# Performance work log

Measured on AMD Instinct MI355X. Metric: run time of the kernel, lower is better.

## Reference

```python
import jax, jax.numpy as jnp
import numpy as np

B, L, H, R, T = 2, 128, 768, 4, 3


def setup_inputs() -> dict:
    key = jax.random.key(0)
    ks = jax.random.split(key, 10)
    s = lambda k, shape: jax.random.normal(k, shape, dtype=jnp.float32) * 0.02
    return {
        "hidden_state": jax.random.normal(ks[0], (B, L, H), dtype=jnp.float32),
        "W_src": s(ks[1], (R * H, H)),
        "b_src": s(ks[2], (R * H,)),
        "W_tgt": s(ks[3], (R * H, H)),
        "b_tgt": s(ks[4], (R * H,)),
        "w_out": s(ks[5], (H,)),
        "dense_W": s(ks[6], (T * H, H)),
        "dense_b": s(ks[7], (T * H,)),
        "clf_W": s(ks[8], (1, H)),
        "clf_b": s(ks[9], (1,)),
    }


def reference(hidden_state, W_src, b_src, W_tgt, b_tgt, w_out,
              dense_W, dense_b, clf_W, clf_b):
    b, l, h = hidden_state.shape
    # Biaffine pairwise relation scoring (dropout = identity at eval).
    h_src = (hidden_state @ W_src.T + b_src).reshape(b, l, R, h)  # [B,L,R,H]
    h_tgt = (hidden_state @ W_tgt.T + b_tgt).reshape(b, l, R, h)  # [B,L,R,H]
    # Pairwise broadcast-add -> tanh -> reduce with w_out. [B,L,L,R,H] intermediate.
    pair = jnp.tanh(h_src[:, :, None, :, :] + h_tgt[:, None, :, :, :])
    relation_logits = jnp.einsum('bstrh,h->bstr', pair, w_out)
    relation_logits = jnp.transpose(relation_logits, (0, 3, 1, 2))  # [B,R,L,L]
    # Token binary classification head.
    z = (hidden_state @ dense_W.T + dense_b).reshape(b, l, T, h)   # [B,L,T,H]
    source_mask_logits = jnp.tanh(z) @ clf_W[0] + clf_b[0]          # [B,L,T]
    source_mask_logits = jnp.transpose(source_mask_logits, (0, 2, 1))  # [B,T,L]
    return relation_logits, source_mask_logits, h_src, h_tgt
```

## Files before the change

### kernel.cpp

```cpp
#include <hip/hip_runtime.h>
#include <hip/hip_bf16.h>

#define LL 128
#define HH 768
#define OFF_REL  0
#define OFF_MASK 131072
#define OFF_HSRC 131840
#define OFF_HTGT 918272
#define SCALEC 2.8853900817779268f

typedef __attribute__((ext_vector_type(8))) short short8;
typedef __attribute__((ext_vector_type(4))) float floatx4;

__device__ inline unsigned short f2bf(float f) {
  unsigned u = __float_as_uint(f);
  u += 0x7FFFu + ((u >> 16) & 1u);
  return (unsigned short)(u >> 16);
}
struct us4 { unsigned short x, y, z, w; };

__global__ __launch_bounds__(256) void cvt_kernel(
    const float4* __restrict__ hs, const float4* __restrict__ wsrc,
    const float4* __restrict__ wtgt, const float4* __restrict__ wd,
    us4* __restrict__ ab, us4* __restrict__ wb)
{
  const int n0 = 49152;
  const int n1 = n0 + 589824;
  const int n2 = n1 + 589824;
  const int n3 = n2 + 442368;
  int stride = gridDim.x * blockDim.x;
  for (int i = blockIdx.x * blockDim.x + threadIdx.x; i < n3; i += stride) {
    const float4* src; us4* dst;
    if (i < n0)      { src = hs   + i;        dst = ab + i; }
    else if (i < n1) { src = wsrc + (i - n0); dst = wb + (i - n0); }
    else if (i < n2) { src = wtgt + (i - n1); dst = wb + 589824 + (i - n1); }
    else             { src = wd   + (i - n2); dst = wb + 1179648 + (i - n2); }
    float4 v = *src;
    us4 o; o.x = f2bf(v.x); o.y = f2bf(v.y); o.z = f2bf(v.z); o.w = f2bf(v.w);
    *dst = o;
  }
}

__global__ __launch_bounds__(256, 4) void gemm_kernel(
    const unsigned short* __restrict__ Ab, const unsigned short* __restrict__ Wb,
    const float* __restrict__ b_src, const float* __restrict__ b_tgt,
    const float* __restrict__ dense_b,
    float* __restrict__ out, float* __restrict__ z,
    float* __restrict__ Es, float* __restrict__ Et)
{
  __shared__ unsigned short sA[2][64][72];
  __shared__ unsigned short sB[2][64][72];
  int tid = threadIdx.x;
  int wave = tid >> 6, lane = tid & 63;
  int nb = blockIdx.x, rb = blockIdx.y;
  int gcol0 = nb * 64;
  int grow0 = rb * 64;

  int s_row = tid >> 3, s_slot = (tid & 7) * 8;
  const unsigned short* gA0 = Ab + (long)(grow0 + s_row) * HH + s_slot;
  const unsigned short* gA1 = gA0 + 32 * HH;
  const unsigned short* gB0 = Wb + (long)(gcol0 + s_row) * HH + s_slot;
  const unsigned short* gB1 = gB0 + 32 * HH;

  int lr = lane & 15, lk8 = (lane >> 4) * 8;
  int wm = (wave >> 1) * 32, wn = (wave & 1) * 32;

  floatx4 acc[2][2];
  #pragma unroll
  for (int mi = 0; mi < 2; ++mi)
    #pragma unroll
    for (int ni = 0; ni < 2; ++ni)
      acc[mi][ni] = (floatx4){0.f, 0.f, 0.f, 0.f};

  {
    uint4 a0 = *(const uint4*)(gA0);
    uint4 a1 = *(const uint4*)(gA1);
    uint4 b0 = *(const uint4*)(gB0);
    uint4 b1 = *(const uint4*)(gB1);
    *(uint4*)&sA[0][s_row][s_slot]      = a0;
    *(uint4*)&sA[0][s_row + 32][s_slot] = a1;
    *(uint4*)&sB[0][s_row][s_slot]      = b0;
    *(uint4*)&sB[0][s_row + 32][s_slot] = b1;
  }
  __syncthreads();

  #pragma unroll 2
  for (int kt = 0; kt < 12; ++kt) {
    int c = kt & 1;
    uint4 na0, na1, nb0, nb1;
    if (kt < 11) {
      int off = (kt + 1) * 64;
      na0 = *(const uint4*)(gA0 + off);
      na1 = *(const uint4*)(gA1 + off);
      nb0 = *(const uint4*)(gB0 + off);
      nb1 = *(const uint4*)(gB1 + off);
    }
    #pragma unroll
    for (int ks = 0; ks < 2; ++ks) {
      short8 fa0 = *(const short8*)&sA[c][wm + lr][ks * 32 + lk8];
      short8 fa1 = *(const short8*)&sA[c][wm + 16 + lr][ks * 32 + lk8];
      short8 fb0 = *(const short8*)&sB[c][wn + lr][ks * 32 + lk8];
      short8 fb1 = *(const short8*)&sB[c][wn + 16 + lr][ks * 32 + lk8];
      acc[0][0] = __builtin_amdgcn_mfma_f32_16x16x32_bf16(fa0, fb0, acc[0][0], 0, 0, 0);
      acc[0][1] = __builtin_amdgcn_mfma_f32_16x16x32_bf16(fa0, fb1, acc[0][1], 0, 0, 0);
      acc[1][0] = __builtin_amdgcn_mfma_f32_16x16x32_bf16(fa1, fb0, acc[1][0], 0, 0, 0);
      acc[1][1] = __builtin_amdgcn_mfma_f32_16x16x32_bf16(fa1, fb1, acc[1][1], 0, 0, 0);
    }
    if (kt < 11) {
      *(uint4*)&sA[c ^ 1][s_row][s_slot]      = na0;
      *(uint4*)&sA[c ^ 1][s_row + 32][s_slot] = na1;
      *(uint4*)&sB[c ^ 1][s_row][s_slot]      = nb0;
      *(uint4*)&sB[c ^ 1][s_row + 32][s_slot] = nb1;
    }
    __syncthreads();
  }

  int lrow = (lane >> 4) * 4;
  #pragma unroll
  for (int mi = 0; mi < 2; ++mi)
  #pragma unroll
  for (int ni = 0; ni < 2; ++ni) {
    int colg = gcol0 + wn + ni * 16 + lr;
    int row0 = grow0 + wm + mi * 16 + lrow;
    if (nb < 48) {
      float bv = b_src[colg];
      #pragma unroll
      for (int r2 = 0; r2 < 4; ++r2) {
        int row = row0 + r2;
        float v = acc[mi][ni][r2] + bv;
        out[OFF_HSRC + row * 3072 + colg] = v;
        Es[row * 3072 + colg] = __builtin_amdgcn_exp2f(SCALEC * v);
      }
    } else if (nb < 96) {
      int cc = colg - 3072;
      float bv = b_tgt[cc];
      #pragma unroll
      for (int r2 = 0; r2 < 4; ++r2) {
        int row = row0 + r2;
        float v = acc[mi][ni][r2] + bv;
        out[OFF_HTGT + row * 3072 + cc] = v;
        Et[row * 3072 + cc] = __builtin_amdgcn_exp2f(SCALEC * v);
      }
    } else {
      int cc = colg - 6144;
      float bv = dense_b[cc];
      #pragma unroll
      for (int r2 = 0; r2 < 4; ++r2)
        z[(row0 + r2) * 2304 + cc] = acc[mi][ni][r2] + bv;
    }
  }
}

#define PHC 256
__global__ __launch_bounds__(512) void pair_kernel(
    const float* __restrict__ Es, const float* __restrict__ Et,
    const float* __restrict__ w_out,
    const float* __restrict__ z, const float* __restrict__ clf_W,
    const float* __restrict__ clf_b, float* __restrict__ out)
{
  int tid = threadIdx.x;

  if (blockIdx.z == 8) {
    int blk = blockIdx.y * 8 + blockIdx.x;
    int wave = tid >> 6, lane = tid & 63;
    int slot = blk * 8 + wave;
    for (int o = slot; o < 768; o += 512) {
      int b = o / 384, rem = o - b * 384;
      int t = rem >> 7, lt = rem & 127;
      const float* zr = z + (long)(b * LL + lt) * 2304 + t * HH;
      float acc = 0.f;
      for (int h = lane; h < HH; h += 64) {
        float x = zr[h];
        float th = 1.f - 2.f * __builtin_amdgcn_rcpf(1.f + __builtin_amdgcn_exp2f(SCALEC * x));
        acc = fmaf(clf_W[h], th, acc);
      }
      #pragma unroll
      for (int d = 32; d; d >>= 1) acc += __shfl_down(acc, d);
      if (lane == 0) out[OFF_MASK + o] = acc + clf_b[0];
    }
    return;
  }

  __shared__ float sA[16][PHC + 4];
  __shared__ float sB[16][PHC + 4];
  __shared__ float sRed[2048];
  __shared__ float sWsum;

  int g = tid >> 6, lane = tid & 63;
  int sq = lane >> 3, tq = lane & 7;
  int t0 = blockIdx.x * 16, s0 = blockIdx.y * 16;
  int br = blockIdx.z, bb = br >> 2, r = br & 3;

  if (tid < 64) {
    float wsm = 0.f;
    for (int h = tid; h < HH; h += 64) wsm += w_out[h];
    #pragma unroll
    for (int d = 32; d; d >>= 1) wsm += __shfl_down(wsm, d);
    if (tid == 0) sWsum = wsm;
  }

  float a00 = 0.f, a01 = 0.f, a10 = 0.f, a11 = 0.f;

  for (int c = 0; c < HH; c += PHC) {
    int offu = __builtin_amdgcn_readfirstlane(c + g * 32);
    float4 wv[8];
    #pragma unroll
    for (int q = 0; q < 8; ++q) wv[q] = *(const float4*)(w_out + offu + q * 4);

    __syncthreads();
    #pragma unroll
    for (int j = 0; j < 2; ++j) {
      int idx = tid * 2 + j;
      int row = idx >> 6, col4 = (idx & 63) * 4;
      *(float4*)&sA[row][col4] =
          *(const float4*)(Es + (long)(bb * LL + s0 + row) * 3072 + r * HH + c + col4);
      *(float4*)&sB[row][col4] =
          *(const float4*)(Et + (long)(bb * LL + t0 + row) * 3072 + r * HH + c + col4);
    }
    __syncthreads();

    const float* pA0 = &sA[2 * sq][g * 32];
    const float* pA1 = &sA[2 * sq + 1][g * 32];
    const float* pB0 = &sB[2 * tq][g * 32];
    const float* pB1 = &sB[2 * tq + 1][g * 32];
    #pragma unroll
    for (int hh = 0; hh < 32; hh += 4) {
      float4 e0 = *(const float4*)(pA0 + hh);
      float4 e1 = *(const float4*)(pA1 + hh);
      float4 f0 = *(const float4*)(pB0 + hh);
      float4 f1 = *(const float4*)(pB1 + hh);
      float4 vw = wv[hh >> 2];
      a00 = fmaf(vw.x, __builtin_amdgcn_rcpf(fmaf(e0.x, f0.x, 1.f)), a00);
      a01 = fmaf(vw.x, __builtin_amdgcn_rcpf(fmaf(e0.x, f1.x, 1.f)), a01);
      a10 = fmaf(vw.x, __builtin_amdgcn_rcpf(fmaf(e1.x, f0.x, 1.f)), a10);
      a11 = fmaf(vw.x, __builtin_amdgcn_rcpf(fmaf(e1.x, f1.x, 1.f)), a11);
      a00 = fmaf(vw.y, __builtin_amdgcn_rcpf(fmaf(e0.y, f0.y, 1.f)), a00);
      a01 = fmaf(vw.y, __builtin_amdgcn_rcpf(fmaf(e0.y, f1.y, 1.f)), a01);
      a10 = fmaf(vw.y, __builtin_amdgcn_rcpf(fmaf(e1.y, f0.y, 1.f)), a10);
      a11 = fmaf(vw.y, __builtin_amdgcn_rcpf(fmaf(e1.y, f1.y, 1.f)), a11);
      a00 = fmaf(vw.z, __builtin_amdgcn_rcpf(fmaf(e0.z, f0.z, 1.f)), a00);
      a01 = fmaf(vw.z, __builtin_amdgcn_rcpf(fmaf(e0.z, f1.z, 1.f)), a01);
      a10 = fmaf(vw.z, __builtin_amdgcn_rcpf(fmaf(e1.z, f0.z, 1.f)), a10);
      a11 = fmaf(vw.z, __builtin_amdgcn_rcpf(fmaf(e1.z, f1.z, 1.f)), a11);
      a00 = fmaf(vw.w, __builtin_amdgcn_rcpf(fmaf(e0.w, f0.w, 1.f)), a00);
      a01 = fmaf(vw.w, __builtin_amdgcn_rcpf(fmaf(e0.w, f1.w, 1.f)), a01);
      a10 = fmaf(vw.w, __builtin_amdgcn_rcpf(fmaf(e1.w, f0.w, 1.f)), a10);
      a11 = fmaf(vw.w, __builtin_amdgcn_rcpf(fmaf(e1.w, f1.w, 1.f)), a11);
    }
  }

  sRed[0 * 512 + g * 64 + lane] = a00;
  sRed[1 * 512 + g * 64 + lane] = a01;
  sRed[2 * 512 + g * 64 + lane] = a10;
  sRed[3 * 512 + g * 64 + lane] = a11;
  __syncthreads();
  if (tid < 256) {
    int s = tid >> 4, t = tid & 15;
    int pp = (s >> 1) * 8 + (t >> 1);
    int sl = (s & 1) * 2 + (t & 1);
    float sum = 0.f;
    #pragma unroll
    for (int gg = 0; gg < 8; ++gg) sum += sRed[sl * 512 + gg * 64 + pp];
    out[((long)br * LL + (s0 + s)) * LL + (t0 + t)] = sWsum - 2.f * sum;
  }
}

extern "C" void kernel_launch(void* const* d_in, const int* in_sizes, int n_in,
                              void* d_out, int out_size, void* d_ws, size_t ws_size,
                              hipStream_t stream)
{
  const float* hidden  = (const float*)d_in[0];
  const float* W_src   = (const float*)d_in[1];
  const float* b_src   = (const float*)d_in[2];
  const float* W_tgt   = (const float*)d_in[3];
  const float* b_tgt   = (const float*)d_in[4];
  const float* w_out   = (const float*)d_in[5];
  const float* dense_W = (const float*)d_in[6];
  const float* dense_b = (const float*)d_in[7];
  const float* clf_W   = (const float*)d_in[8];
  const float* clf_b   = (const float*)d_in[9];
  float* out = (float*)d_out;
  char* ws = (char*)d_ws;

  unsigned short* Ab = (unsigned short*)ws;
  unsigned short* Wb = (unsigned short*)(ws + 393216);
  float* z  = (float*)(ws + 13369344);
  float* Es = (float*)(ws + 15728640);
  float* Et = (float*)(ws + 18874368);

  hipLaunchKernelGGL(cvt_kernel, dim3(2048), dim3(256), 0, stream,
      (const float4*)hidden, (const float4*)W_src, (const float4*)W_tgt,
      (const float4*)dense_W, (us4*)Ab, (us4*)Wb);
  hipLaunchKernelGGL(gemm_kernel, dim3(132, 4), dim3(256), 0, stream,
      Ab, Wb, b_src, b_tgt, dense_b, out, z, Es, Et);
  hipLaunchKernelGGL(pair_kernel, dim3(8, 8, 9), dim3(512), 0, stream,
      Es, Et, w_out, z, clf_W, clf_b, out + OFF_REL);
}
```

Measured before the change: 44.63 us.

## Fuse fp32-to-bf16 conversion into GEMM tile loads, drop the separate convert kernel

Removes the standalone conversion kernel that wrote bf16 copies of the hidden state and all three weight matrices. The GEMM now reads fp32 directly from global memory and converts to bf16 while staging tiles into shared memory. This saves a launch and a full extra write and read of about 13 MB of weights. In exchange each GEMM tile load moves twice as many bytes and holds more registers for the prefetched fp32 values, which may affect occupancy. The hidden-state rows are also reconverted by every column block.

```diff
diff --git a/kernel.cpp b/kernel.cpp
--- a/kernel.cpp
+++ b/kernel.cpp
@@ -12,37 +12,19 @@
 typedef __attribute__((ext_vector_type(8))) short short8;
 typedef __attribute__((ext_vector_type(4))) float floatx4;
 
-__device__ inline unsigned short f2bf(float f) {
-  unsigned u = __float_as_uint(f);
-  u += 0x7FFFu + ((u >> 16) & 1u);
-  return (unsigned short)(u >> 16);
-}
-struct us4 { unsigned short x, y, z, w; };
-
-__global__ __launch_bounds__(256) void cvt_kernel(
-    const float4* __restrict__ hs, const float4* __restrict__ wsrc,
-    const float4* __restrict__ wtgt, const float4* __restrict__ wd,
-    us4* __restrict__ ab, us4* __restrict__ wb)
-{
-  const int n0 = 49152;
-  const int n1 = n0 + 589824;
-  const int n2 = n1 + 589824;
-  const int n3 = n2 + 442368;
-  int stride = gridDim.x * blockDim.x;
-  for (int i = blockIdx.x * blockDim.x + threadIdx.x; i < n3; i += stride) {
-    const float4* src; us4* dst;
-    if (i < n0)      { src = hs   + i;        dst = ab + i; }
-    else if (i < n1) { src = wsrc + (i - n0); dst = wb + (i - n0); }
-    else if (i < n2) { src = wtgt + (i - n1); dst = wb + 589824 + (i - n1); }
-    else             { src = wd   + (i - n2); dst = wb + 1179648 + (i - n2); }
-    float4 v = *src;
-    us4 o; o.x = f2bf(v.x); o.y = f2bf(v.y); o.z = f2bf(v.z); o.w = f2bf(v.w);
-    *dst = o;
-  }
+__device__ __forceinline__ uint4 cvt8(float4 lo, float4 hi) {
+  union { __hip_bfloat162 h2[4]; uint4 u4; } u;
+  u.h2[0] = __float22bfloat162_rn(float2{lo.x, lo.y});
+  u.h2[1] = __float22bfloat162_rn(float2{lo.z, lo.w});
+  u.h2[2] = __float22bfloat162_rn(float2{hi.x, hi.y});
+  u.h2[3] = __float22bfloat162_rn(float2{hi.z, hi.w});
+  return u.u4;
 }
 
 __global__ __launch_bounds__(256, 4) void gemm_kernel(
-    const unsigned short* __restrict__ Ab, const unsigned short* __restrict__ Wb,
+    const float* __restrict__ hidden,
+    const float* __restrict__ Wsrc, const float* __restrict__ Wtgt,
+    const float* __restrict__ Wd,
     const float* __restrict__ b_src, const float* __restrict__ b_tgt,
     const float* __restrict__ dense_b,
     float* __restrict__ out, float* __restrict__ z,
@@ -56,11 +38,16 @@
   int gcol0 = nb * 64;
   int grow0 = rb * 64;
 
+  const float* W; int wrow0; int which;
+  if (nb < 48)      { W = Wsrc; wrow0 = gcol0;        which = 0; }
+  else if (nb < 96) { W = Wtgt; wrow0 = gcol0 - 3072; which = 1; }
+  else              { W = Wd;   wrow0 = gcol0 - 6144; which = 2; }
+
   int s_row = tid >> 3, s_slot = (tid & 7) * 8;
-  const unsigned short* gA0 = Ab + (long)(grow0 + s_row) * HH + s_slot;
-  const unsigned short* gA1 = gA0 + 32 * HH;
-  const unsigned short* gB0 = Wb + (long)(gcol0 + s_row) * HH + s_slot;
-  const unsigned short* gB1 = gB0 + 32 * HH;
+  const float* gA0 = hidden + (long)(grow0 + s_row) * HH + s_slot;
+  const float* gA1 = gA0 + 32 * HH;
+  const float* gB0 = W + (long)(wrow0 + s_row) * HH + s_slot;
+  const float* gB1 = gB0 + 32 * HH;
 
   int lr = lane & 15, lk8 = (lane >> 4) * 8;
   int wm = (wave >> 1) * 32, wn = (wave & 1) * 32;
@@ -73,27 +60,27 @@
       acc[mi][ni] = (floatx4){0.f, 0.f, 0.f, 0.f};
 
   {
-    uint4 a0 = *(const uint4*)(gA0);
-    uint4 a1 = *(const uint4*)(gA1);
-    uint4 b0 = *(const uint4*)(gB0);
-    uint4 b1 = *(const uint4*)(gB1);
-    *(uint4*)&sA[0][s_row][s_slot]      = a0;
-    *(uint4*)&sA[0][s_row + 32][s_slot] = a1;
-    *(uint4*)&sB[0][s_row][s_slot]      = b0;
-    *(uint4*)&sB[0][s_row + 32][s_slot] = b1;
+    float4 a0l = *(const float4*)(gA0),     a0h = *(const float4*)(gA0 + 4);
+    float4 a1l = *(const float4*)(gA1),     a1h = *(const float4*)(gA1 + 4);
+    float4 b0l = *(const float4*)(gB0),     b0h = *(const float4*)(gB0 + 4);
+    float4 b1l = *(const float4*)(gB1),     b1h = *(const float4*)(gB1 + 4);
+    *(uint4*)&sA[0][s_row][s_slot]      = cvt8(a0l, a0h);
+    *(uint4*)&sA[0][s_row + 32][s_slot] = cvt8(a1l, a1h);
+    *(uint4*)&sB[0][s_row][s_slot]      = cvt8(b0l, b0h);
+    *(uint4*)&sB[0][s_row + 32][s_slot] = cvt8(b1l, b1h);
   }
   __syncthreads();
 
   #pragma unroll 2
   for (int kt = 0; kt < 12; ++kt) {
     int c = kt & 1;
-    uint4 na0, na1, nb0, nb1;
+    float4 na0l, na0h, na1l, na1h, nb0l, nb0h, nb1l, nb1h;
     if (kt < 11) {
       int off = (kt + 1) * 64;
-      na0 = *(const uint4*)(gA0 + off);
-      na1 = *(const uint4*)(gA1 + off);
-      nb0 = *(const uint4*)(gB0 + off);
-      nb1 = *(const uint4*)(gB1 + off);
+      na0l = *(const float4*)(gA0 + off); na0h = *(const float4*)(gA0 + off + 4);
+      na1l = *(const float4*)(gA1 + off); na1h = *(const float4*)(gA1 + off + 4);
+      nb0l = *(const float4*)(gB0 + off); nb0h = *(const float4*)(gB0 + off + 4);
+      nb1l = *(const float4*)(gB1 + off); nb1h = *(const float4*)(gB1 + off + 4);
     }
     #pragma unroll
     for (int ks = 0; ks < 2; ++ks) {
@@ -107,10 +94,10 @@
       acc[1][1] = __builtin_amdgcn_mfma_f32_16x16x32_bf16(fa1, fb1, acc[1][1], 0, 0, 0);
     }
     if (kt < 11) {
-      *(uint4*)&sA[c ^ 1][s_row][s_slot]      = na0;
-      *(uint4*)&sA[c ^ 1][s_row + 32][s_slot] = na1;
-      *(uint4*)&sB[c ^ 1][s_row][s_slot]      = nb0;
-      *(uint4*)&sB[c ^ 1][s_row + 32][s_slot] = nb1;
+      *(uint4*)&sA[c ^ 1][s_row][s_slot]      = cvt8(na0l, na0h);
+      *(uint4*)&sA[c ^ 1][s_row + 32][s_slot] = cvt8(na1l, na1h);
+      *(uint4*)&sB[c ^ 1][s_row][s_slot]      = cvt8(nb0l, nb0h);
+      *(uint4*)&sB[c ^ 1][s_row + 32][s_slot] = cvt8(nb1l, nb1h);
     }
     __syncthreads();
   }
@@ -122,7 +109,7 @@
   for (int ni = 0; ni < 2; ++ni) {
     int colg = gcol0 + wn + ni * 16 + lr;
     int row0 = grow0 + wm + mi * 16 + lrow;
-    if (nb < 48) {
+    if (which == 0) {
       float bv = b_src[colg];
       #pragma unroll
       for (int r2 = 0; r2 < 4; ++r2) {
@@ -131,7 +118,7 @@
         out[OFF_HSRC + row * 3072 + colg] = v;
         Es[row * 3072 + colg] = __builtin_amdgcn_exp2f(SCALEC * v);
       }
-    } else if (nb < 96) {
+    } else if (which == 1) {
       int cc = colg - 3072;
       float bv = b_tgt[cc];
       #pragma unroll
@@ -282,17 +269,12 @@
   float* out = (float*)d_out;
   char* ws = (char*)d_ws;
 
-  unsigned short* Ab = (unsigned short*)ws;
-  unsigned short* Wb = (unsigned short*)(ws + 393216);
-  float* z  = (float*)(ws + 13369344);
-  float* Es = (float*)(ws + 15728640);
-  float* Et = (float*)(ws + 18874368);
-
-  hipLaunchKernelGGL(cvt_kernel, dim3(2048), dim3(256), 0, stream,
-      (const float4*)hidden, (const float4*)W_src, (const float4*)W_tgt,
-      (const float4*)dense_W, (us4*)Ab, (us4*)Wb);
+  float* z  = (float*)(ws);
+  float* Es = (float*)(ws + 2359296);
+  float* Et = (float*)(ws + 5505024);
+
   hipLaunchKernelGGL(gemm_kernel, dim3(132, 4), dim3(256), 0, stream,
-      Ab, Wb, b_src, b_tgt, dense_b, out, z, Es, Et);
+      hidden, W_src, W_tgt, dense_W, b_src, b_tgt, dense_b, out, z, Es, Et);
   hipLaunchKernelGGL(pair_kernel, dim3(8, 8, 9), dim3(512), 0, stream,
       Es, Et, w_out, z, clf_W, clf_b, out + OFF_REL);
 }
```

Measured after the change: 44.39 us. No clear change (-0.5%).

## Use direct global-to-LDS loads and 128-row tiles in projection GEMM

Applied to the files above, without the earlier changes.

Rewrites the projection GEMM to stage A and B tiles with global_load_lds, which writes global memory straight into shared memory without passing through registers. The M tile grows from 64 to 128 rows and the K step shrinks to 32, so each wave computes a 64x32 output with eight MFMAs per step and the grid halves to 132x2 blocks. The goal is to cut register traffic and redundant weight loads. In exchange the LDS layout is unpadded (64-byte rows), which may cause bank conflicts, the loop needs twice as many barriers, and fewer blocks may leave CUs idle.

```diff
diff --git a/kernel.cpp b/kernel.cpp
--- a/kernel.cpp
+++ b/kernel.cpp
@@ -18,6 +18,13 @@
   return (unsigned short)(u >> 16);
 }
 struct us4 { unsigned short x, y, z, w; };
+
+__device__ __forceinline__ void gload16(const void* g, void* l) {
+  __builtin_amdgcn_global_load_lds(
+      (const __attribute__((address_space(1))) unsigned int*)g,
+      (__attribute__((address_space(3))) unsigned int*)l,
+      16, 0, 0);
+}
 
 __global__ __launch_bounds__(256) void cvt_kernel(
     const float4* __restrict__ hs, const float4* __restrict__ wsrc,
@@ -48,96 +55,87 @@
     float* __restrict__ out, float* __restrict__ z,
     float* __restrict__ Es, float* __restrict__ Et)
 {
-  __shared__ unsigned short sA[2][64][72];
-  __shared__ unsigned short sB[2][64][72];
+  __shared__ __align__(1024) unsigned short sAB[2][6144];
   int tid = threadIdx.x;
   int wave = tid >> 6, lane = tid & 63;
-  int nb = blockIdx.x, rb = blockIdx.y;
+  int nb = blockIdx.x;
+  int mb = blockIdx.y * 128;
+
+  int which = (nb < 48) ? 0 : (nb < 96) ? 1 : 2;
   int gcol0 = nb * 64;
-  int grow0 = rb * 64;
-
-  int s_row = tid >> 3, s_slot = (tid & 7) * 8;
-  const unsigned short* gA0 = Ab + (long)(grow0 + s_row) * HH + s_slot;
-  const unsigned short* gA1 = gA0 + 32 * HH;
-  const unsigned short* gB0 = Wb + (long)(gcol0 + s_row) * HH + s_slot;
-  const unsigned short* gB1 = gB0 + 32 * HH;
-
-  int lr = lane & 15, lk8 = (lane >> 4) * 8;
-  int wm = (wave >> 1) * 32, wn = (wave & 1) * 32;
-
-  floatx4 acc[2][2];
+
+  int srowA = wave * 16 + (lane >> 2);
+  int sslot = (lane & 3) * 8;
+  const unsigned short* gA = Ab + (long)(mb + srowA) * HH + sslot;
+  const unsigned short* gB = Wb + (long)(gcol0 + srowA) * HH + sslot;
+
+  int lr = lane & 15;
+  int lk16 = (lane >> 4) * 16;
+  int wm = (wave >> 1) * 64, wn = (wave & 1) * 32;
+
+  floatx4 acc[4][2];
   #pragma unroll
-  for (int mi = 0; mi < 2; ++mi)
-    #pragma unroll
-    for (int ni = 0; ni < 2; ++ni)
-      acc[mi][ni] = (floatx4){0.f, 0.f, 0.f, 0.f};
-
-  {
-    uint4 a0 = *(const uint4*)(gA0);
-    uint4 a1 = *(const uint4*)(gA1);
-    uint4 b0 = *(const uint4*)(gB0);
-    uint4 b1 = *(const uint4*)(gB1);
-    *(uint4*)&sA[0][s_row][s_slot]      = a0;
-    *(uint4*)&sA[0][s_row + 32][s_slot] = a1;
-    *(uint4*)&sB[0][s_row][s_slot]      = b0;
-    *(uint4*)&sB[0][s_row + 32][s_slot] = b1;
-  }
+  for (int fi = 0; fi < 4; ++fi)
+    #pragma unroll
+    for (int fj = 0; fj < 2; ++fj)
+      acc[fi][fj] = (floatx4){0.f, 0.f, 0.f, 0.f};
+
+#define STAGE(BUF, KT) do {                                              \
+    char* base = (char*)&sAB[BUF][0];                                    \
+    gload16(gA + (KT) * 32,            base + wave * 1024);              \
+    gload16(gA + 64 * HH + (KT) * 32,  base + 4096 + wave * 1024);       \
+    gload16(gB + (KT) * 32,            base + 8192 + wave * 1024);       \
+  } while (0)
+
+  STAGE(0, 0);
   __syncthreads();
 
   #pragma unroll 2
-  for (int kt = 0; kt < 12; ++kt) {
-    int c = kt & 1;
-    uint4 na0, na1, nb0, nb1;
-    if (kt < 11) {
-      int off = (kt + 1) * 64;
-      na0 = *(const uint4*)(gA0 + off);
-      na1 = *(const uint4*)(gA1 + off);
-      nb0 = *(const uint4*)(gB0 + off);
-      nb1 = *(const uint4*)(gB1 + off);
-    }
-    #pragma unroll
-    for (int ks = 0; ks < 2; ++ks) {
-      short8 fa0 = *(const short8*)&sA[c][wm + lr][ks * 32 + lk8];
-      short8 fa1 = *(const short8*)&sA[c][wm + 16 + lr][ks * 32 + lk8];
-      short8 fb0 = *(const short8*)&sB[c][wn + lr][ks * 32 + lk8];
-      short8 fb1 = *(const short8*)&sB[c][wn + 16 + lr][ks * 32 + lk8];
-      acc[0][0] = __builtin_amdgcn_mfma_f32_16x16x32_bf16(fa0, fb0, acc[0][0], 0, 0, 0);
-      acc[0][1] = __builtin_amdgcn_mfma_f32_16x16x32_bf16(fa0, fb1, acc[0][1], 0, 0, 0);
-      acc[1][0] = __builtin_amdgcn_mfma_f32_16x16x32_bf16(fa1, fb0, acc[1][0], 0, 0, 0);
-      acc[1][1] = __builtin_amdgcn_mfma_f32_16x16x32_bf16(fa1, fb1, acc[1][1], 0, 0, 0);
-    }
-    if (kt < 11) {
-      *(uint4*)&sA[c ^ 1][s_row][s_slot]      = na0;
-      *(uint4*)&sA[c ^ 1][s_row + 32][s_slot] = na1;
-      *(uint4*)&sB[c ^ 1][s_row][s_slot]      = nb0;
-      *(uint4*)&sB[c ^ 1][s_row + 32][s_slot] = nb1;
-    }
+  for (int kt = 0; kt < 24; ++kt) {
+    int cur = kt & 1;
+    if (kt < 23) STAGE(cur ^ 1, kt + 1);
+    const char* base = (const char*)&sAB[cur][0];
+    short8 af0 = *(const short8*)(base + (wm + lr) * 64 + lk16);
+    short8 af1 = *(const short8*)(base + (wm + 16 + lr) * 64 + lk16);
+    short8 af2 = *(const short8*)(base + (wm + 32 + lr) * 64 + lk16);
+    short8 af3 = *(const short8*)(base + (wm + 48 + lr) * 64 + lk16);
+    short8 bf0 = *(const short8*)(base + 8192 + (wn + lr) * 64 + lk16);
+    short8 bf1 = *(const short8*)(base + 8192 + (wn + 16 + lr) * 64 + lk16);
+    acc[0][0] = __builtin_amdgcn_mfma_f32_16x16x32_bf16(af0, bf0, acc[0][0], 0, 0, 0);
+    acc[0][1] = __builtin_amdgcn_mfma_f32_16x16x32_bf16(af0, bf1, acc[0][1], 0, 0, 0);
+    acc[1][0] = __builtin_amdgcn_mfma_f32_16x16x32_bf16(af1, bf0, acc[1][0], 0, 0, 0);
+    acc[1][1] = __builtin_amdgcn_mfma_f32_16x16x32_bf16(af1, bf1, acc[1][1], 0, 0, 0);
+    acc[2][0] = __builtin_amdgcn_mfma_f32_16x16x32_bf16(af2, bf0, acc[2][0], 0, 0, 0);
+    acc[2][1] = __builtin_amdgcn_mfma_f32_16x16x32_bf16(af2, bf1, acc[2][1], 0, 0, 0);
+    acc[3][0] = __builtin_amdgcn_mfma_f32_16x16x32_bf16(af3, bf0, acc[3][0], 0, 0, 0);
+    acc[3][1] = __builtin_amdgcn_mfma_f32_16x16x32_bf16(af3, bf1, acc[3][1], 0, 0, 0);
     __syncthreads();
   }
+#undef STAGE
 
   int lrow = (lane >> 4) * 4;
   #pragma unroll
-  for (int mi = 0; mi < 2; ++mi)
+  for (int fi = 0; fi < 4; ++fi)
   #pragma unroll
-  for (int ni = 0; ni < 2; ++ni) {
-    int colg = gcol0 + wn + ni * 16 + lr;
-    int row0 = grow0 + wm + mi * 16 + lrow;
-    if (nb < 48) {
+  for (int fj = 0; fj < 2; ++fj) {
+    int colg = gcol0 + wn + fj * 16 + lr;
+    int row0 = mb + wm + fi * 16 + lrow;
+    if (which == 0) {
       float bv = b_src[colg];
       #pragma unroll
       for (int r2 = 0; r2 < 4; ++r2) {
         int row = row0 + r2;
-        float v = acc[mi][ni][r2] + bv;
+        float v = acc[fi][fj][r2] + bv;
         out[OFF_HSRC + row * 3072 + colg] = v;
         Es[row * 3072 + colg] = __builtin_amdgcn_exp2f(SCALEC * v);
       }
-    } else if (nb < 96) {
+    } else if (which == 1) {
       int cc = colg - 3072;
       float bv = b_tgt[cc];
       #pragma unroll
       for (int r2 = 0; r2 < 4; ++r2) {
         int row = row0 + r2;
-        float v = acc[mi][ni][r2] + bv;
+        float v = acc[fi][fj][r2] + bv;
         out[OFF_HTGT + row * 3072 + cc] = v;
         Et[row * 3072 + cc] = __builtin_amdgcn_exp2f(SCALEC * v);
       }
@@ -146,7 +144,7 @@
       float bv = dense_b[cc];
       #pragma unroll
       for (int r2 = 0; r2 < 4; ++r2)
-        z[(row0 + r2) * 2304 + cc] = acc[mi][ni][r2] + bv;
+        z[(row0 + r2) * 2304 + cc] = acc[fi][fj][r2] + bv;
     }
   }
 }
@@ -291,7 +289,7 @@
   hipLaunchKernelGGL(cvt_kernel, dim3(2048), dim3(256), 0, stream,
       (const float4*)hidden, (const float4*)W_src, (const float4*)W_tgt,
       (const float4*)dense_W, (us4*)Ab, (us4*)Wb);
-  hipLaunchKernelGGL(gemm_kernel, dim3(132, 4), dim3(256), 0, stream,
+  hipLaunchKernelGGL(gemm_kernel, dim3(132, 2), dim3(256), 0, stream,
       Ab, Wb, b_src, b_tgt, dense_b, out, z, Es, Et);
   hipLaunchKernelGGL(pair_kernel, dim3(8, 8, 9), dim3(512), 0, stream,
       Es, Et, w_out, z, clf_W, clf_b, out + OFF_REL);
```

Result: slower. 46.36 us (+3.9%).

## Load MFMA fragments directly from global memory, dropping LDS staging in GEMM

Applied to the files above, without the earlier changes.

Drops the shared-memory double-buffered tiles from the projection GEMM. Each wave now loads its bf16 A/B fragments straight from global memory into registers with a one-step register prefetch. This removes LDS writes and reads plus block barriers. In exchange, data shared between waves is no longer reused through LDS, so global/L2 traffic rises (each fragment row is fetched by two waves) and the 16-byte per-lane row-strided loads are less coalesced.

```diff
diff --git a/kernel.cpp b/kernel.cpp
--- a/kernel.cpp
+++ b/kernel.cpp
@@ -48,23 +48,21 @@
     float* __restrict__ out, float* __restrict__ z,
     float* __restrict__ Es, float* __restrict__ Et)
 {
-  __shared__ unsigned short sA[2][64][72];
-  __shared__ unsigned short sB[2][64][72];
   int tid = threadIdx.x;
   int wave = tid >> 6, lane = tid & 63;
   int nb = blockIdx.x, rb = blockIdx.y;
   int gcol0 = nb * 64;
   int grow0 = rb * 64;
-
-  int s_row = tid >> 3, s_slot = (tid & 7) * 8;
-  const unsigned short* gA0 = Ab + (long)(grow0 + s_row) * HH + s_slot;
-  const unsigned short* gA1 = gA0 + 32 * HH;
-  const unsigned short* gB0 = Wb + (long)(gcol0 + s_row) * HH + s_slot;
-  const unsigned short* gB1 = gB0 + 32 * HH;
+  int which = (nb < 48) ? 0 : (nb < 96) ? 1 : 2;
 
   int lr = lane & 15, lk8 = (lane >> 4) * 8;
   int wm = (wave >> 1) * 32, wn = (wave & 1) * 32;
 
+  const unsigned short* gA0 = Ab + (long)(grow0 + wm + lr) * HH + lk8;
+  const unsigned short* gA1 = gA0 + 16 * HH;
+  const unsigned short* gB0 = Wb + (long)(gcol0 + wn + lr) * HH + lk8;
+  const unsigned short* gB1 = gB0 + 16 * HH;
+
   floatx4 acc[2][2];
   #pragma unroll
   for (int mi = 0; mi < 2; ++mi)
@@ -72,47 +70,26 @@
     for (int ni = 0; ni < 2; ++ni)
       acc[mi][ni] = (floatx4){0.f, 0.f, 0.f, 0.f};
 
-  {
-    uint4 a0 = *(const uint4*)(gA0);
-    uint4 a1 = *(const uint4*)(gA1);
-    uint4 b0 = *(const uint4*)(gB0);
-    uint4 b1 = *(const uint4*)(gB1);
-    *(uint4*)&sA[0][s_row][s_slot]      = a0;
-    *(uint4*)&sA[0][s_row + 32][s_slot] = a1;
-    *(uint4*)&sB[0][s_row][s_slot]      = b0;
-    *(uint4*)&sB[0][s_row + 32][s_slot] = b1;
-  }
-  __syncthreads();
-
-  #pragma unroll 2
-  for (int kt = 0; kt < 12; ++kt) {
-    int c = kt & 1;
-    uint4 na0, na1, nb0, nb1;
-    if (kt < 11) {
-      int off = (kt + 1) * 64;
-      na0 = *(const uint4*)(gA0 + off);
-      na1 = *(const uint4*)(gA1 + off);
-      nb0 = *(const uint4*)(gB0 + off);
-      nb1 = *(const uint4*)(gB1 + off);
-    }
-    #pragma unroll
-    for (int ks = 0; ks < 2; ++ks) {
-      short8 fa0 = *(const short8*)&sA[c][wm + lr][ks * 32 + lk8];
-      short8 fa1 = *(const short8*)&sA[c][wm + 16 + lr][ks * 32 + lk8];
-      short8 fb0 = *(const short8*)&sB[c][wn + lr][ks * 32 + lk8];
-      short8 fb1 = *(const short8*)&sB[c][wn + 16 + lr][ks * 32 + lk8];
-      acc[0][0] = __builtin_amdgcn_mfma_f32_16x16x32_bf16(fa0, fb0, acc[0][0], 0, 0, 0);
-      acc[0][1] = __builtin_amdgcn_mfma_f32_16x16x32_bf16(fa0, fb1, acc[0][1], 0, 0, 0);
-      acc[1][0] = __builtin_amdgcn_mfma_f32_16x16x32_bf16(fa1, fb0, acc[1][0], 0, 0, 0);
-      acc[1][1] = __builtin_amdgcn_mfma_f32_16x16x32_bf16(fa1, fb1, acc[1][1], 0, 0, 0);
-    }
-    if (kt < 11) {
-      *(uint4*)&sA[c ^ 1][s_row][s_slot]      = na0;
-      *(uint4*)&sA[c ^ 1][s_row + 32][s_slot] = na1;
-      *(uint4*)&sB[c ^ 1][s_row][s_slot]      = nb0;
-      *(uint4*)&sB[c ^ 1][s_row + 32][s_slot] = nb1;
-    }
-    __syncthreads();
+  short8 a0 = *(const short8*)(gA0);
+  short8 a1 = *(const short8*)(gA1);
+  short8 b0 = *(const short8*)(gB0);
+  short8 b1 = *(const short8*)(gB1);
+
+  #pragma unroll
+  for (int kt = 0; kt < 24; ++kt) {
+    short8 na0, na1, nb0, nb1;
+    if (kt < 23) {
+      int off = (kt + 1) * 32;
+      na0 = *(const short8*)(gA0 + off);
+      na1 = *(const short8*)(gA1 + off);
+      nb0 = *(const short8*)(gB0 + off);
+      nb1 = *(const short8*)(gB1 + off);
+    }
+    acc[0][0] = __builtin_amdgcn_mfma_f32_16x16x32_bf16(a0, b0, acc[0][0], 0, 0, 0);
+    acc[0][1] = __builtin_amdgcn_mfma_f32_16x16x32_bf16(a0, b1, acc[0][1], 0, 0, 0);
+    acc[1][0] = __builtin_amdgcn_mfma_f32_16x16x32_bf16(a1, b0, acc[1][0], 0, 0, 0);
+    acc[1][1] = __builtin_amdgcn_mfma_f32_16x16x32_bf16(a1, b1, acc[1][1], 0, 0, 0);
+    a0 = na0; a1 = na1; b0 = nb0; b1 = nb1;
   }
 
   int lrow = (lane >> 4) * 4;
@@ -122,7 +99,7 @@
   for (int ni = 0; ni < 2; ++ni) {
     int colg = gcol0 + wn + ni * 16 + lr;
     int row0 = grow0 + wm + mi * 16 + lrow;
-    if (nb < 48) {
+    if (which == 0) {
       float bv = b_src[colg];
       #pragma unroll
       for (int r2 = 0; r2 < 4; ++r2) {
@@ -131,7 +108,7 @@
         out[OFF_HSRC + row * 3072 + colg] = v;
         Es[row * 3072 + colg] = __builtin_amdgcn_exp2f(SCALEC * v);
       }
-    } else if (nb < 96) {
+    } else if (which == 1) {
       int cc = colg - 3072;
       float bv = b_tgt[cc];
       #pragma unroll
```

New measurement: 67.06 us (median of 2 runs). 50.3% more time.
